# Optimization experiments

Measured on AMD Instinct MI355X. Metric: run time of the kernel, lower is better.

The kernel has to match this reference:

```python
import jax, jax.numpy as jnp
import numpy as np

NUM_CLASSES = 100
EPS = 1e-07


def setup_inputs() -> dict:
    key = jax.random.key(0)
    k1, k2 = jax.random.split(key)
    N = 1_000_000
    logits = jax.random.normal(k1, (N, NUM_CLASSES), dtype=jnp.float32)
    labels = jax.random.randint(k2, (N,), 0, NUM_CLASSES, dtype=jnp.int32)
    return {"logits": logits, "labels": labels}


def reference(logits, labels):
    # pred: [N] argmax class per sample
    pred = jnp.argmax(logits, axis=1)
    C = NUM_CLASSES
    zeros = jnp.zeros((C,), dtype=jnp.float32)
    # single-pass confusion-matrix marginals (replaces per-class python loop)
    pred_count = zeros.at[pred].add(1.0)          # tp_c + fp_c
    true_count = zeros.at[labels].add(1.0)        # tp_c + fn_c
    correct = (pred == labels).astype(jnp.float32)
    tp = zeros.at[labels].add(correct)            # tp_c
    fp = pred_count - tp
    fn = true_count - tp
    precision = tp / (tp + fp + EPS)
    recall = tp / (tp + fn + EPS)
    # beta = 1 -> (1 + 1) * p * r / (1 * p + r + eps)
    f1 = 2.0 * precision * recall / (precision + recall + EPS)
    return jnp.mean(f1)
```

## Files before the change

### kernel.cpp

```cpp
#include <hip/hip_runtime.h>

#define NCLS 100
#define EPS 1e-7f

__global__ void zero_counts_kernel(unsigned int* __restrict__ counts) {
    int i = threadIdx.x;
    if (i < 3 * NCLS) counts[i] = 0u;
}

__global__ __launch_bounds__(256) void hist_kernel(
        const float* __restrict__ logits,
        const int* __restrict__ labels,
        unsigned int* __restrict__ counts,
        int N) {
    __shared__ unsigned int s_pred[NCLS];
    __shared__ unsigned int s_true[NCLS];
    __shared__ unsigned int s_tp[NCLS];
    for (int i = threadIdx.x; i < NCLS; i += blockDim.x) {
        s_pred[i] = 0u; s_true[i] = 0u; s_tp[i] = 0u;
    }
    __syncthreads();

    const int stride = gridDim.x * blockDim.x;
    for (int row = blockIdx.x * blockDim.x + threadIdx.x; row < N; row += stride) {
        const float4* p = (const float4*)(logits + (size_t)row * NCLS);
        float best = -INFINITY;
        int bi = 0;
        #pragma unroll
        for (int j = 0; j < NCLS / 4; ++j) {
            float4 v = p[j];
            int c = j * 4;
            if (v.x > best) { best = v.x; bi = c;     }
            if (v.y > best) { best = v.y; bi = c + 1; }
            if (v.z > best) { best = v.z; bi = c + 2; }
            if (v.w > best) { best = v.w; bi = c + 3; }
        }
        int lab = labels[row];
        atomicAdd(&s_pred[bi], 1u);
        atomicAdd(&s_true[lab], 1u);
        if (bi == lab) atomicAdd(&s_tp[lab], 1u);
    }

    __syncthreads();
    for (int i = threadIdx.x; i < NCLS; i += blockDim.x) {
        unsigned int v;
        if ((v = s_pred[i]) != 0u) atomicAdd(&counts[i], v);
        if ((v = s_true[i]) != 0u) atomicAdd(&counts[NCLS + i], v);
        if ((v = s_tp[i])   != 0u) atomicAdd(&counts[2 * NCLS + i], v);
    }
}

__global__ void finalize_kernel(const unsigned int* __restrict__ counts,
                                float* __restrict__ out) {
    __shared__ float s_f1[NCLS];
    int c = threadIdx.x;
    if (c < NCLS) {
        float tp    = (float)counts[2 * NCLS + c];
        float predc = (float)counts[c];
        float truec = (float)counts[NCLS + c];
        float fp = predc - tp;
        float fn = truec - tp;
        float precision = tp / (tp + fp + EPS);
        float recall    = tp / (tp + fn + EPS);
        float f1 = 2.0f * precision * recall / (precision + recall + EPS);
        s_f1[c] = f1;
    }
    __syncthreads();
    if (c == 0) {
        float sum = 0.0f;
        for (int i = 0; i < NCLS; ++i) sum += s_f1[i];
        out[0] = sum / (float)NCLS;
    }
}

extern "C" void kernel_launch(void* const* d_in, const int* in_sizes, int n_in,
                              void* d_out, int out_size, void* d_ws, size_t ws_size,
                              hipStream_t stream) {
    const float* logits = (const float*)d_in[0];
    const int*   labels = (const int*)d_in[1];
    float* out = (float*)d_out;
    unsigned int* counts = (unsigned int*)d_ws;

    const int N = in_sizes[1];

    zero_counts_kernel<<<1, 320, 0, stream>>>(counts);

    const int block = 256;
    const int grid  = 2048;
    hist_kernel<<<grid, block, 0, stream>>>(logits, labels, counts, N);

    finalize_kernel<<<1, 128, 0, stream>>>(counts, out);
}
```

Baseline: 622.6 us.

## Split each row's argmax across four lanes with shuffle reduction

Assigns four consecutive lanes to each row so that lane q reads every fourth float4 of the row, and combines partial maxima with xor shuffles, breaking ties toward the lower index. Adjacent lanes now read adjacent 16-byte chunks instead of addresses 400 bytes apart, which improves coalescing. All loads are issued before any comparisons, raising the number of memory requests in flight. In exchange it adds shuffle work and leaves three of every four lanes idle during the atomics.

```diff
diff --git a/kernel.cpp b/kernel.cpp
--- a/kernel.cpp
+++ b/kernel.cpp
@@ -21,24 +21,51 @@
     }
     __syncthreads();
 
-    const int stride = gridDim.x * blockDim.x;
-    for (int row = blockIdx.x * blockDim.x + threadIdx.x; row < N; row += stride) {
+    const int tid    = blockIdx.x * blockDim.x + threadIdx.x;
+    const int q      = tid & 3;
+    const int quad   = tid >> 2;
+    const int nquads = (gridDim.x * blockDim.x) >> 2;
+
+    for (int row = quad; row < N; row += nquads) {
         const float4* p = (const float4*)(logits + (size_t)row * NCLS);
+
+        float4 v[7];
+        #pragma unroll
+        for (int k = 0; k < 6; ++k) v[k] = p[4 * k + q];
+        if (q == 0) v[6] = p[24];
+
         float best = -INFINITY;
-        int bi = 0;
+        int bidx = 0;
         #pragma unroll
-        for (int j = 0; j < NCLS / 4; ++j) {
-            float4 v = p[j];
-            int c = j * 4;
-            if (v.x > best) { best = v.x; bi = c;     }
-            if (v.y > best) { best = v.y; bi = c + 1; }
-            if (v.z > best) { best = v.z; bi = c + 2; }
-            if (v.w > best) { best = v.w; bi = c + 3; }
+        for (int k = 0; k < 6; ++k) {
+            const int c = (4 * k + q) * 4;
+            float4 w = v[k];
+            if (w.x > best) { best = w.x; bidx = c;     }
+            if (w.y > best) { best = w.y; bidx = c + 1; }
+            if (w.z > best) { best = w.z; bidx = c + 2; }
+            if (w.w > best) { best = w.w; bidx = c + 3; }
         }
-        int lab = labels[row];
-        atomicAdd(&s_pred[bi], 1u);
-        atomicAdd(&s_true[lab], 1u);
-        if (bi == lab) atomicAdd(&s_tp[lab], 1u);
+        if (q == 0) {
+            float4 w = v[6];
+            if (w.x > best) { best = w.x; bidx = 96; }
+            if (w.y > best) { best = w.y; bidx = 97; }
+            if (w.z > best) { best = w.z; bidx = 98; }
+            if (w.w > best) { best = w.w; bidx = 99; }
+        }
+
+        #pragma unroll
+        for (int m = 1; m <= 2; m <<= 1) {
+            float ob = __shfl_xor(best, m, 64);
+            int   oi = __shfl_xor(bidx, m, 64);
+            if (ob > best || (ob == best && oi < bidx)) { best = ob; bidx = oi; }
+        }
+
+        if (q == 0) {
+            int lab = labels[row];
+            atomicAdd(&s_pred[bidx], 1u);
+            atomicAdd(&s_true[lab], 1u);
+            if (bidx == lab) atomicAdd(&s_tp[lab], 1u);
+        }
     }
 
     __syncthreads();
```

Measured after the change: 532.4 us. -14.5%, faster.
